# Performance work log

Hardware: AMD Instinct MI355X
Metric: run time of the kernel (lower is better)

## Reference

```python
import jax, jax.numpy as jnp
import numpy as np

E = 1024
H = 16
HD = E // H
FF = 4 * E
B, T = 2, 2048


def _linear_params(key, fan_in, fan_out):
    k1, k2 = jax.random.split(key)
    bound = 1.0 / np.sqrt(fan_in)
    W = jax.random.uniform(k1, (fan_out, fan_in), jnp.float32, -bound, bound)
    b = jax.random.uniform(k2, (fan_out,), jnp.float32, -bound, bound)
    return W, b


def setup_inputs() -> dict:
    key = jax.random.key(0)
    keys = jax.random.split(key, 8)
    x = jax.random.normal(keys[0], (B, T, E), jnp.float32)
    Wq, bq = _linear_params(keys[1], E, E)
    Wk, bk = _linear_params(keys[2], E, E)
    Wv, bv = _linear_params(keys[3], E, E)
    Wo, bo = _linear_params(keys[4], E, E)
    W1, b1 = _linear_params(keys[5], E, FF)
    W2, b2 = _linear_params(keys[6], FF, E)
    ln1_g = jnp.ones((E,), jnp.float32); ln1_b = jnp.zeros((E,), jnp.float32)
    ln2_g = jnp.ones((E,), jnp.float32); ln2_b = jnp.zeros((E,), jnp.float32)
    return {"x": x, "Wq": Wq, "bq": bq, "Wk": Wk, "bk": bk, "Wv": Wv, "bv": bv,
            "Wo": Wo, "bo": bo, "W1": W1, "b1": b1, "W2": W2, "b2": b2,
            "ln1_g": ln1_g, "ln1_b": ln1_b, "ln2_g": ln2_g, "ln2_b": ln2_b}


def _layernorm(x, g, b, eps=1e-5):
    mu = jnp.mean(x, axis=-1, keepdims=True)
    var = jnp.var(x, axis=-1, keepdims=True)
    return (x - mu) * jax.lax.rsqrt(var + eps) * g + b


def reference(x, Wq, bq, Wk, bk, Wv, bv, Wo, bo, W1, b1, W2, b2,
              ln1_g, ln1_b, ln2_g, ln2_b):
    Bc, Tc, Ec = x.shape
    h = _layernorm(x, ln1_g, ln1_b)
    # projections (torch Linear: y = x @ W.T + b)
    q = (h @ Wq.T + bq).reshape(Bc, Tc, H, HD).transpose(0, 2, 1, 3)  # [B,H,T,hd]
    k = (h @ Wk.T + bk).reshape(Bc, Tc, H, HD).transpose(0, 2, 1, 3)
    v = (h @ Wv.T + bv).reshape(Bc, Tc, H, HD).transpose(0, 2, 1, 3)
    scores = jnp.einsum('bhqd,bhkd->bhqk', q, k) / np.sqrt(HD).astype(np.float32)
    causal = jnp.tril(jnp.ones((Tc, Tc), bool))
    scores = jnp.where(causal, scores, -jnp.inf)
    att = jax.nn.softmax(scores, axis=-1)  # dropout = identity (eval)
    out = jnp.einsum('bhqk,bhkd->bhqd', att, v)
    out = out.transpose(0, 2, 1, 3).reshape(Bc, Tc, Ec)
    x = x + out @ Wo.T + bo
    h2 = _layernorm(x, ln2_g, ln2_b)
    ff = jax.nn.relu(h2 @ W1.T + b1) @ W2.T + b2
    return x + ff
```

## Files before the change

### kernel.cpp

```cpp
#include <hip/hip_runtime.h>

typedef unsigned short u16;
typedef __bf16 bf16x8 __attribute__((ext_vector_type(8)));
typedef float f32x4 __attribute__((ext_vector_type(4)));

#define E_ 1024
#define T_ 2048
#define B_ 2
#define H_ 16
#define FF_ 4096
#define M_ 4096

__device__ __forceinline__ u16 f2b(float f) {
    union { float f; unsigned u; } c; c.f = f;
    unsigned r = c.u + 0x7FFFu + ((c.u >> 16) & 1u);
    return (u16)(r >> 16);
}
__device__ __forceinline__ u16 f2bt(float f) {
    union { float f; unsigned u; } c; c.f = f;
    return (u16)(c.u >> 16);
}

__device__ __forceinline__ void gl16(const u16* g, u16* l) {
    __builtin_amdgcn_global_load_lds(
        (__attribute__((address_space(1))) void*)g,
        (__attribute__((address_space(3))) void*)l, 16, 0, 0);
}

template<int N> __device__ __forceinline__ void wait_vmcnt() {
    if constexpr (N == 2)      asm volatile("s_waitcnt vmcnt(2)" ::: "memory");
    else if constexpr (N == 3) asm volatile("s_waitcnt vmcnt(3)" ::: "memory");
    else if constexpr (N == 4) asm volatile("s_waitcnt vmcnt(4)" ::: "memory");
    else                       asm volatile("s_waitcnt vmcnt(0)" ::: "memory");
}

__global__ __launch_bounds__(256) void cvt_ln(
        const float* __restrict__ Wq, const float* __restrict__ Wk,
        const float* __restrict__ Wv, const float* __restrict__ Wo,
        const float* __restrict__ W1, const float* __restrict__ W2,
        const float* __restrict__ bq, const float* __restrict__ bk,
        const float* __restrict__ bv,
        u16* __restrict__ WqkvB, u16* __restrict__ WoB,
        u16* __restrict__ W1B, u16* __restrict__ W2B,
        float* __restrict__ bqkv,
        const float* __restrict__ x, const float* __restrict__ g1,
        const float* __restrict__ b1v, u16* __restrict__ hB) {
    if (blockIdx.x < 1024) {
        int row = blockIdx.x * 4 + (threadIdx.x >> 6);
        int t = threadIdx.x & 63;
        const float* xr = x + (size_t)row * E_;
        float v[16];
        float sum = 0.f, ss = 0.f;
#pragma unroll
        for (int c = 0; c < 4; c++) {
            float4 f = *(const float4*)&xr[c * 256 + t * 4];
            v[c * 4 + 0] = f.x; v[c * 4 + 1] = f.y; v[c * 4 + 2] = f.z; v[c * 4 + 3] = f.w;
            sum += f.x + f.y + f.z + f.w;
            ss += f.x * f.x + f.y * f.y + f.z * f.z + f.w * f.w;
        }
#pragma unroll
        for (int d = 32; d; d >>= 1) {
            sum += __shfl_xor(sum, d);
            ss  += __shfl_xor(ss, d);
        }
        float mu = sum * (1.f / E_);
        float var = ss * (1.f / E_) - mu * mu;
        float rs = rsqrtf(var + 1e-5f);
#pragma unroll
        for (int c = 0; c < 4; c++) {
            int idx = c * 256 + t * 4;
            float4 g4 = *(const float4*)&g1[idx];
            float4 b4 = *(const float4*)&b1v[idx];
            ushort4 o;
            o.x = f2b((v[c * 4 + 0] - mu) * rs * g4.x + b4.x);
            o.y = f2b((v[c * 4 + 1] - mu) * rs * g4.y + b4.y);
            o.z = f2b((v[c * 4 + 2] - mu) * rs * g4.z + b4.z);
            o.w = f2b((v[c * 4 + 3] - mu) * rs * g4.w + b4.w);
            *(ushort4*)&hB[(size_t)row * E_ + idx] = o;
        }
        return;
    }
    int i = (blockIdx.x - 1024) * 256 + threadIdx.x;
    if (i >= 3146496) return;
    if (i >= 3145728) {
        int j = i - 3145728;
        const float* s = (j < 256) ? bq : (j < 512) ? bk : bv;
        int jj = j & 255;
        *(float4*)&bqkv[j * 4] = *(const float4*)&s[jj * 4];
        return;
    }
    const float* src; u16* dst; int j;
    if (i < 786432) {
        src = (i < 262144) ? Wq : (i < 524288) ? Wk : Wv;
        j = i & 262143;
        dst = WqkvB + (i >> 18) * (E_ * E_);
    } else if (i < 1048576) { j = i - 786432;  src = Wo; dst = WoB; }
    else if (i < 2097152)   { j = i - 1048576; src = W1; dst = W1B; }
    else                    { j = i - 2097152; src = W2; dst = W2B; }
    float4 f = *(const float4*)&src[j * 4];
    ushort4 o;
    o.x = f2b(f.x); o.y = f2b(f.y); o.z = f2b(f.z); o.w = f2b(f.w);
    *(ushort4*)&dst[j * 4] = o;
}

__global__ __launch_bounds__(64) void ln_fwd(u16* __restrict__ out, const float* __restrict__ x,
                                             const float* __restrict__ g, const float* __restrict__ bta) {
    int row = blockIdx.x;
    int t = threadIdx.x;
    const float* xr = x + (size_t)row * E_;
    float v[16];
    float sum = 0.f, ss = 0.f;
#pragma unroll
    for (int c = 0; c < 4; c++) {
        float4 f = *(const float4*)&xr[c * 256 + t * 4];
        v[c * 4 + 0] = f.x; v[c * 4 + 1] = f.y; v[c * 4 + 2] = f.z; v[c * 4 + 3] = f.w;
        sum += f.x + f.y + f.z + f.w;
        ss += f.x * f.x + f.y * f.y + f.z * f.z + f.w * f.w;
    }
#pragma unroll
    for (int d = 32; d; d >>= 1) {
        sum += __shfl_xor(sum, d);
        ss  += __shfl_xor(ss, d);
    }
    float mu = sum * (1.f / E_);
    float var = ss * (1.f / E_) - mu * mu;
    float rs = rsqrtf(var + 1e-5f);
#pragma unroll
    for (int c = 0; c < 4; c++) {
        int idx = c * 256 + t * 4;
        float4 g4 = *(const float4*)&g[idx];
        float4 b4 = *(const float4*)&bta[idx];
        ushort4 o;
        o.x = f2b((v[c * 4 + 0] - mu) * rs * g4.x + b4.x);
        o.y = f2b((v[c * 4 + 1] - mu) * rs * g4.y + b4.y);
        o.z = f2b((v[c * 4 + 2] - mu) * rs * g4.z + b4.z);
        o.w = f2b((v[c * 4 + 3] - mu) * rs * g4.w + b4.w);
        *(ushort4*)&out[(size_t)row * E_ + idx] = o;
    }
}

template<int BM, int BN>
__global__ __launch_bounds__(256) void gemm_bt(
        const u16* __restrict__ A, const u16* __restrict__ Bt,
        const float* __restrict__ bias, const float* __restrict__ residual,
        float* __restrict__ outF, float* __restrict__ oP1,
        float* __restrict__ oP2, float* __restrict__ oP3,
        u16* __restrict__ outB, u16* __restrict__ outVt,
        int M, int N, int K, int ldk, int relu, int qkvmode, int swz) {
    constexpr int MT = BM / 32, NT = BN / 32;
    constexpr int LA = BM / 64, LB = BN / 64;
    __shared__ __align__(16) u16 As[3][BM * 32];
    __shared__ __align__(16) u16 Bs[3][BN * 32];
    int tid = threadIdx.x;
    int bx = blockIdx.x, by = blockIdx.y;
    if (swz) {
        int gx = gridDim.x;
        int nwg = gx * gridDim.y;
        int lin = by * gx + bx;
        int w = (lin & 7) * (nwg >> 3) + (lin >> 3);
        bx = w % gx; by = w / gx;
    }
    int m0 = by * BM, n0 = bx * BN;
    int kz = blockIdx.z;
    int koff = kz * K;
    int wave = tid >> 6, lane = tid & 63;
    int wm = wave & 1, wn = wave >> 1;
    int r16 = lane & 15, kg = lane >> 4;

    const u16* gA = A + (size_t)(m0 + wave * (BM / 4) + (lane >> 2)) * ldk + koff + (lane & 3) * 8;
    const u16* gB = Bt + (size_t)(n0 + wave * (BN / 4) + (lane >> 2)) * ldk + koff + (lane & 3) * 8;
    size_t row16 = (size_t)16 * ldk;
    int aoff = wave * (BM / 4) * 32;
    int boff = wave * (BN / 4) * 32;

    f32x4 acc[MT][NT] = {};

    const int nk = K >> 5;

    auto issue = [&](int kt, int buf) {
        int k1 = kt << 5;
        gl16(gA + k1, As[buf] + aoff);
        if (LA == 2) gl16(gA + k1 + row16, As[buf] + aoff + 512);
        gl16(gB + k1, Bs[buf] + boff);
        if (LB == 2) gl16(gB + k1 + row16, Bs[buf] + boff + 512);
    };

    auto compute = [&](int cb) {
        bf16x8 af[MT], bfr[NT];
#pragma unroll
        for (int mt = 0; mt < MT; mt++)
            af[mt] = *(const bf16x8*)&As[cb][(wm * (BM / 2) + mt * 16 + r16) * 32 + kg * 8];
#pragma unroll
        for (int nt = 0; nt < NT; nt++)
            bfr[nt] = *(const bf16x8*)&Bs[cb][(wn * (BN / 2) + nt * 16 + r16) * 32 + kg * 8];
#pragma unroll
        for (int mt = 0; mt < MT; mt++)
#pragma unroll
            for (int nt = 0; nt < NT; nt++)
                acc[mt][nt] = __builtin_amdgcn_mfma_f32_16x16x32_bf16(af[mt], bfr[nt], acc[mt][nt], 0, 0, 0);
    };

    issue(0, 0);
    issue(1, 1);

    int cur = 0;
    for (int ks = 0; ks < nk - 1; ks++) {
        wait_vmcnt<LA + LB>();
        __builtin_amdgcn_s_barrier();
        asm volatile("" ::: "memory");
        if (ks + 2 < nk) {
            int p2 = cur ? cur - 1 : 2;
            issue(ks + 2, p2);
        }
        compute(cur);
        cur = (cur < 2) ? cur + 1 : 0;
    }
    asm volatile("s_waitcnt vmcnt(0)" ::: "memory");
    __builtin_amdgcn_s_barrier();
    asm volatile("" ::: "memory");
    compute(cur);

#pragma unroll
    for (int mt = 0; mt < MT; mt++) {
#pragma unroll
        for (int nt = 0; nt < NT; nt++) {
            int gm = m0 + wm * (BM / 2) + mt * 16 + kg * 4;
            int gn = n0 + wn * (BN / 2) + nt * 16 + r16;
            float bv = bias[gn];
            if (qkvmode) {
                if (gn < 2048) {
                    float scl = (gn < 1024) ? 0.18033688f : 1.0f;
#pragma unroll
                    for (int r = 0; r < 4; r++)
                        outB[(size_t)(gm + r) * 2048 + gn] = f2b((acc[mt][nt][r] + bv) * scl);
                } else {
                    int bq_ = gm >> 11, tq = gm & 2047, d = gn - 2048;
                    ushort4 ov;
                    ov.x = f2b(acc[mt][nt][0] + bv);
                    ov.y = f2b(acc[mt][nt][1] + bv);
                    ov.z = f2b(acc[mt][nt][2] + bv);
                    ov.w = f2b(acc[mt][nt][3] + bv);
                    *(ushort4*)&outVt[((size_t)(bq_ * 1024 + d)) * 2048 + tq] = ov;
                }
            } else if (oP1) {
                float* po = (kz == 1) ? oP1 : (kz == 2) ? oP2 : oP3;
#pragma unroll
                for (int r = 0; r < 4; r++) {
                    size_t off = (size_t)(gm + r) * N + gn;
                    if (kz == 0) {
                        float v = acc[mt][nt][r] + bv;
                        if (residual) v += residual[off];
                        outF[off] = v;
                    } else {
                        po[off] = acc[mt][nt][r];
                    }
                }
            } else {
#pragma unroll
                for (int r = 0; r < 4; r++) {
                    float v = acc[mt][nt][r] + bv;
                    size_t off = (size_t)(gm + r) * N + gn;
                    if (residual) v += residual[off];
                    if (relu) v = fmaxf(v, 0.f);
                    if (outF) outF[off] = v;
                    else outB[off] = f2b(v);
                }
            }
        }
    }
}

__global__ __launch_bounds__(256) void addf3(float* __restrict__ d, const float* __restrict__ a,
                                             const float* __restrict__ b, const float* __restrict__ c) {
    size_t i = ((size_t)blockIdx.x * 256 + threadIdx.x) * 4;
    float4 vd = *(float4*)&d[i];
    float4 va = *(const float4*)&a[i];
    float4 vb = *(const float4*)&b[i];
    float4 vc = *(const float4*)&c[i];
    vd.x += va.x + vb.x + vc.x;
    vd.y += va.y + vb.y + vc.y;
    vd.z += va.z + vb.z + vc.z;
    vd.w += va.w + vb.w + vc.w;
    *(float4*)&d[i] = vd;
}

#define AST 68
__global__ __launch_bounds__(256) void attn_mfma(
        const u16* __restrict__ qk, const u16* __restrict__ vt,
        u16* __restrict__ out) {
    __shared__ __align__(16) u16 Ks[2][64 * AST];
    __shared__ __align__(16) u16 Vs[2][64 * AST];
    __shared__ __align__(16) u16 Ps[4][16 * AST];

    int bz = blockIdx.x;
    int h  = bz & 15;
    int b  = (bz >> 4) & 1;
    int qt = bz >> 5;

    int tid = threadIdx.x;
    int w = tid >> 6, lane = tid & 63;
    int g = lane >> 4, l16 = lane & 15;

    int qrow = qt * 64 + w * 16 + l16;
    bf16x8 qf[2];
    qf[0] = *(const bf16x8*)&qk[(size_t)(b * T_ + qrow) * 2048 + h * 64 + g * 8];
    qf[1] = *(const bf16x8*)&qk[(size_t)(b * T_ + qrow) * 2048 + h * 64 + 32 + g * 8];

    f32x4 o[4] = {};
    f32x4 lp = {0.f, 0.f, 0.f, 0.f};

    int r1 = tid >> 3, col1 = (tid & 7) * 8;
    const u16* gK = qk + (size_t)(b * T_) * 2048 + 1024 + h * 64;
    const u16* gV = vt + (size_t)(b * 1024 + h * 64) * 2048;

    uint4 kr1 = *(const uint4*)&gK[(size_t)r1 * 2048 + col1];
    uint4 kr2 = *(const uint4*)&gK[(size_t)(r1 + 32) * 2048 + col1];
    uint4 vr1 = *(const uint4*)&gV[(size_t)r1 * 2048 + col1];
    uint4 vr2 = *(const uint4*)&gV[(size_t)(r1 + 32) * 2048 + col1];

    for (int t = 0; t <= qt; t++) {
        int cur = t & 1;
        *(uint4*)&Ks[cur][r1 * AST + col1] = kr1;
        *(uint4*)&Ks[cur][(r1 + 32) * AST + col1] = kr2;
        *(uint4*)&Vs[cur][r1 * AST + col1] = vr1;
        *(uint4*)&Vs[cur][(r1 + 32) * AST + col1] = vr2;
        __syncthreads();
        if (t < qt) {
            int j1 = (t + 1) * 64;
            kr1 = *(const uint4*)&gK[(size_t)(j1 + r1) * 2048 + col1];
            kr2 = *(const uint4*)&gK[(size_t)(j1 + r1 + 32) * 2048 + col1];
            vr1 = *(const uint4*)&gV[(size_t)r1 * 2048 + j1 + col1];
            vr2 = *(const uint4*)&gV[(size_t)(r1 + 32) * 2048 + j1 + col1];
        }

        f32x4 s[4];
#pragma unroll
        for (int nt = 0; nt < 4; nt++) {
            f32x4 c16 = {-16.f, -16.f, -16.f, -16.f};
            bf16x8 k0 = *(const bf16x8*)&Ks[cur][(nt * 16 + l16) * AST + g * 8];
            bf16x8 k1 = *(const bf16x8*)&Ks[cur][(nt * 16 + l16) * AST + 32 + g * 8];
            s[nt] = __builtin_amdgcn_mfma_f32_16x16x32_bf16(qf[0], k0, c16, 0, 0, 0);
            s[nt] = __builtin_amdgcn_mfma_f32_16x16x32_bf16(qf[1], k1, s[nt], 0, 0, 0);
        }

        if (t == qt) {
            int j0 = t * 64;
#pragma unroll
            for (int nt = 0; nt < 4; nt++) {
                int key = j0 + nt * 16 + l16;
#pragma unroll
                for (int r = 0; r < 4; r++) {
                    int q = qt * 64 + w * 16 + g * 4 + r;
                    if (key > q) s[nt][r] = -INFINITY;
                }
            }
        }

#pragma unroll
        for (int nt = 0; nt < 4; nt++)
#pragma unroll
            for (int r = 0; r < 4; r++) {
                float p = exp2f(s[nt][r]);
                lp[r] += p;
                Ps[w][(g * 4 + r) * AST + nt * 16 + l16] = f2bt(p);
            }

#pragma unroll
        for (int kf = 0; kf < 2; kf++) {
            bf16x8 pf = *(const bf16x8*)&Ps[w][l16 * AST + kf * 32 + g * 8];
#pragma unroll
            for (int nt = 0; nt < 4; nt++) {
                bf16x8 vf = *(const bf16x8*)&Vs[cur][(nt * 16 + l16) * AST + kf * 32 + g * 8];
                o[nt] = __builtin_amdgcn_mfma_f32_16x16x32_bf16(pf, vf, o[nt], 0, 0, 0);
            }
        }
    }

#pragma unroll
    for (int x = 1; x <= 8; x <<= 1)
#pragma unroll
        for (int r = 0; r < 4; r++)
            lp[r] += __shfl_xor(lp[r], x);

    float inv[4];
#pragma unroll
    for (int r = 0; r < 4; r++) inv[r] = 1.f / lp[r];
    int qg = qt * 64 + w * 16 + g * 4;
#pragma unroll
    for (int nt = 0; nt < 4; nt++)
#pragma unroll
        for (int r = 0; r < 4; r++)
            out[(size_t)(b * T_ + qg + r) * E_ + h * 64 + nt * 16 + l16] =
                f2b(o[nt][r] * inv[r]);
}

extern "C" void kernel_launch(void* const* d_in, const int* in_sizes, int n_in,
                              void* d_out, int out_size, void* d_ws, size_t ws_size,
                              hipStream_t stream) {
    const float* x    = (const float*)d_in[0];
    const float* Wq   = (const float*)d_in[1];
    const float* bq   = (const float*)d_in[2];
    const float* Wk   = (const float*)d_in[3];
    const float* bk   = (const float*)d_in[4];
    const float* Wv   = (const float*)d_in[5];
    const float* bv   = (const float*)d_in[6];
    const float* Wo   = (const float*)d_in[7];
    const float* bo   = (const float*)d_in[8];
    const float* W1   = (const float*)d_in[9];
    const float* b1   = (const float*)d_in[10];
    const float* W2   = (const float*)d_in[11];
    const float* b2   = (const float*)d_in[12];
    const float* ln1g = (const float*)d_in[13];
    const float* ln1b = (const float*)d_in[14];
    const float* ln2g = (const float*)d_in[15];
    const float* ln2b = (const float*)d_in[16];

    char* ws = (char*)d_ws;
    size_t off = 0;
    auto alloc = [&](size_t bytes) { char* p = ws + off; off += (bytes + 255) & ~(size_t)255; return p; };

    u16*   hB    = (u16*)  alloc((size_t)M_ * E_ * 2);
    u16*   WqkvB = (u16*)  alloc((size_t)3 * E_ * E_ * 2);
    u16*   WoB   = (u16*)  alloc((size_t)E_ * E_ * 2);
    u16*   W1B   = (u16*)  alloc((size_t)FF_ * E_ * 2);
    u16*   W2B   = (u16*)  alloc((size_t)E_ * FF_ * 2);
    float* bqkv  = (float*)alloc(3 * E_ * 4);
    u16*   qkB   = (u16*)  alloc((size_t)M_ * 2 * E_ * 2);
    u16*   vtG   = (u16*)  alloc((size_t)M_ * E_ * 2);
    u16*   attnB = (u16*)  alloc((size_t)M_ * E_ * 2);
    float* x2    = (float*)alloc((size_t)M_ * E_ * 4);
    u16*   h2B   = (u16*)  alloc((size_t)M_ * E_ * 2);
    u16*   rB    = (u16*)  alloc((size_t)M_ * FF_ * 2);
    float* P1    = (float*)alloc((size_t)M_ * E_ * 4);
    float* P2 = (float*)qkB;
    float* P3 = (float*)ws;

    cvt_ln<<<1024 + 12291, 256, 0, stream>>>(Wq, Wk, Wv, Wo, W1, W2, bq, bk, bv,
                                             WqkvB, WoB, W1B, W2B, bqkv,
                                             x, ln1g, ln1b, hB);

    gemm_bt<128, 128><<<dim3(3 * E_ / 128, M_ / 128), 256, 0, stream>>>(
        hB, WqkvB, bqkv, nullptr, nullptr, nullptr, nullptr, nullptr, qkB, vtG,
        M_, 3 * E_, E_, E_, 0, 1, 0);

    attn_mfma<<<B_ * H_ * (T_ / 64), 256, 0, stream>>>(qkB, vtG, attnB);

    gemm_bt<64, 128><<<dim3(E_ / 128, M_ / 64), 256, 0, stream>>>(
        attnB, WoB, bo, x, x2, nullptr, nullptr, nullptr, nullptr, nullptr,
        M_, E_, E_, E_, 0, 0, 0);

    ln_fwd<<<M_, 64, 0, stream>>>(h2B, x2, ln2g, ln2b);

    gemm_bt<128, 128><<<dim3(FF_ / 128, M_ / 128), 256, 0, stream>>>(
        h2B, W1B, b1, nullptr, nullptr, nullptr, nullptr, nullptr, rB, nullptr,
        M_, FF_, E_, E_, 1, 0, 1);

    gemm_bt<128, 128><<<dim3(E_ / 128, M_ / 128, 4), 256, 0, stream>>>(
        rB, W2B, b2, x2, (float*)d_out, P1, P2, P3, nullptr, nullptr,
        M_, E_, FF_ / 4, FF_, 0, 0, 1);

    addf3<<<(M_ * E_) / (256 * 4), 256, 0, stream>>>((float*)d_out, P1, P2, P3);
}
```

Baseline: 387.3 us.

## Add 256x256-tile 512-thread GEMM kernel for QKV, FFN1 and FFN2

Introduces a new GEMM kernel with 256x256 output tiles, 8 waves, a K-step of 64, XOR-swizzled LDS layout, double-buffered global-to-LDS loads interleaved across four MFMA phases, and raised wave priority during MFMA. The QKV projection, FFN up-projection and split-K FFN down-projection now use it in place of the 128x128 kernel, aiming for more data reuse per tile and better overlap of loads with compute. The larger tiles mean fewer workgroups (for example 192 for QKV and 64 per split for FFN2), which may underfill the GPU's compute units and raises LDS and register pressure.

```diff
diff --git a/kernel.cpp b/kernel.cpp
--- a/kernel.cpp
+++ b/kernel.cpp
@@ -136,6 +136,155 @@
         o.z = f2b((v[c * 4 + 2] - mu) * rs * g4.z + b4.z);
         o.w = f2b((v[c * 4 + 3] - mu) * rs * g4.w + b4.w);
         *(ushort4*)&out[(size_t)row * E_ + idx] = o;
+    }
+}
+
+template<int QKV, int SPLIT>
+__global__ __launch_bounds__(512) void gemm256(
+        const u16* __restrict__ A, const u16* __restrict__ Bt,
+        const float* __restrict__ bias, const float* __restrict__ residual,
+        float* __restrict__ outF, float* __restrict__ oP1,
+        float* __restrict__ oP2, float* __restrict__ oP3,
+        u16* __restrict__ outB, u16* __restrict__ outVt,
+        int N, int K, int ldk, int relu) {
+    __shared__ __align__(16) u16 As[2][256 * 64];
+    __shared__ __align__(16) u16 Bs[2][256 * 64];
+    int tid = threadIdx.x;
+    int bx = blockIdx.x, by = blockIdx.y;
+    {
+        int gx = gridDim.x;
+        int nwg = gx * (int)gridDim.y, cpx = nwg >> 3;
+        int lin = by * gx + bx;
+        int wv = (lin & 7) * cpx + (lin >> 3);
+        bx = wv % gx; by = wv / gx;
+    }
+    int m0 = by * 256, n0 = bx * 256;
+    int kz = blockIdx.z;
+    int koff = kz * K;
+    int w = tid >> 6, lane = tid & 63;
+    int wm = w >> 2, wn = w & 3;
+    int r16 = lane & 15, kg = lane >> 4;
+    int sw = (r16 & 7) << 3;
+
+    int srow = tid >> 3;
+    int schunk = (tid & 7) ^ (srow & 7);
+    const u16* gAs = A + (size_t)(m0 + srow) * ldk + koff + schunk * 8;
+    const u16* gBs = Bt + (size_t)(n0 + srow) * ldk + koff + schunk * 8;
+    size_t rstep = (size_t)64 * ldk;
+
+    f32x4 acc[8][4] = {};
+    const int nk = K >> 6;
+
+    auto stA = [&](int kt, int b, int r0, int r1) {
+        const u16* g = gAs + kt * 64;
+        u16* l = &As[b][0] + tid * 8;
+        gl16(g + (size_t)r0 * rstep, l + r0 * 4096);
+        gl16(g + (size_t)r1 * rstep, l + r1 * 4096);
+    };
+    auto stB = [&](int kt, int b, int r0, int r1) {
+        const u16* g = gBs + kt * 64;
+        u16* l = &Bs[b][0] + tid * 8;
+        gl16(g + (size_t)r0 * rstep, l + r0 * 4096);
+        gl16(g + (size_t)r1 * rstep, l + r1 * 4096);
+    };
+
+    stB(0, 0, 0, 1); stB(0, 0, 2, 3); stA(0, 0, 0, 2); stA(0, 0, 1, 3);
+    asm volatile("s_waitcnt vmcnt(2)" ::: "memory");
+    __builtin_amdgcn_s_barrier();
+    asm volatile("" ::: "memory");
+
+    for (int t = 0; t < nk; t++) {
+        int cb = t & 1, nb = cb ^ 1;
+        const bool pf = (t + 1 < nk);
+        bf16x8 bfr[4];
+#pragma unroll
+        for (int ph = 0; ph < 4; ph++) {
+            const int kk = ph >> 1, mh = ph & 1;
+            int ce = kk * 32 + kg * 8;
+            if (mh == 0) {
+#pragma unroll
+                for (int nf = 0; nf < 4; nf++) {
+                    int row = wn * 64 + nf * 16 + r16;
+                    bfr[nf] = *(const bf16x8*)&Bs[cb][(row * 64 + ce) ^ sw];
+                }
+            }
+            bf16x8 af[4];
+#pragma unroll
+            for (int i = 0; i < 4; i++) {
+                int row = wm * 128 + (mh * 4 + i) * 16 + r16;
+                af[i] = *(const bf16x8*)&As[cb][(row * 64 + ce) ^ sw];
+            }
+            if (pf) {
+                if (ph == 0)      stB(t + 1, nb, 0, 1);
+                else if (ph == 1) stB(t + 1, nb, 2, 3);
+                else if (ph == 2) stA(t + 1, nb, 0, 2);
+                else              stA(t + 1, nb, 1, 3);
+            }
+            __builtin_amdgcn_s_barrier();
+            asm volatile("s_waitcnt lgkmcnt(0)" ::: "memory");
+            __builtin_amdgcn_s_setprio(1);
+#pragma unroll
+            for (int i = 0; i < 4; i++)
+#pragma unroll
+                for (int nf = 0; nf < 4; nf++)
+                    acc[mh * 4 + i][nf] = __builtin_amdgcn_mfma_f32_16x16x32_bf16(
+                        af[i], bfr[nf], acc[mh * 4 + i][nf], 0, 0, 0);
+            __builtin_amdgcn_s_setprio(0);
+            if (ph == 0) {
+                if (pf) asm volatile("s_waitcnt vmcnt(2)" ::: "memory");
+                else    asm volatile("s_waitcnt vmcnt(0)" ::: "memory");
+            } else if (ph == 3 && pf) {
+                asm volatile("s_waitcnt vmcnt(2)" ::: "memory");
+            }
+            __builtin_amdgcn_s_barrier();
+            asm volatile("" ::: "memory");
+        }
+    }
+
+#pragma unroll
+    for (int mf = 0; mf < 8; mf++) {
+#pragma unroll
+        for (int nf = 0; nf < 4; nf++) {
+            int gm = m0 + wm * 128 + mf * 16 + kg * 4;
+            int gn = n0 + wn * 64 + nf * 16 + r16;
+            float bv = bias[gn];
+            if (QKV) {
+                if (gn < 2048) {
+                    float scl = (gn < 1024) ? 0.18033688f : 1.0f;
+#pragma unroll
+                    for (int r = 0; r < 4; r++)
+                        outB[(size_t)(gm + r) * 2048 + gn] = f2b((acc[mf][nf][r] + bv) * scl);
+                } else {
+                    int bq_ = gm >> 11, tq = gm & 2047, d = gn - 2048;
+                    ushort4 ov;
+                    ov.x = f2b(acc[mf][nf][0] + bv);
+                    ov.y = f2b(acc[mf][nf][1] + bv);
+                    ov.z = f2b(acc[mf][nf][2] + bv);
+                    ov.w = f2b(acc[mf][nf][3] + bv);
+                    *(ushort4*)&outVt[((size_t)(bq_ * 1024 + d)) * 2048 + tq] = ov;
+                }
+            } else if (SPLIT) {
+                float* po = (kz == 1) ? oP1 : (kz == 2) ? oP2 : oP3;
+#pragma unroll
+                for (int r = 0; r < 4; r++) {
+                    size_t off = (size_t)(gm + r) * N + gn;
+                    if (kz == 0) {
+                        float v = acc[mf][nf][r] + bv;
+                        if (residual) v += residual[off];
+                        outF[off] = v;
+                    } else {
+                        po[off] = acc[mf][nf][r];
+                    }
+                }
+            } else {
+#pragma unroll
+                for (int r = 0; r < 4; r++) {
+                    float v = acc[mf][nf][r] + bv;
+                    if (relu) v = fmaxf(v, 0.f);
+                    outB[(size_t)(gm + r) * N + gn] = f2b(v);
+                }
+            }
+        }
     }
 }
 
@@ -157,8 +306,8 @@
         int gx = gridDim.x;
         int nwg = gx * gridDim.y;
         int lin = by * gx + bx;
-        int w = (lin & 7) * (nwg >> 3) + (lin >> 3);
-        bx = w % gx; by = w / gx;
+        int wv = (lin & 7) * (nwg >> 3) + (lin >> 3);
+        bx = wv % gx; by = wv / gx;
     }
     int m0 = by * BM, n0 = bx * BN;
     int kz = blockIdx.z;
@@ -439,9 +588,9 @@
                                              WqkvB, WoB, W1B, W2B, bqkv,
                                              x, ln1g, ln1b, hB);
 
-    gemm_bt<128, 128><<<dim3(3 * E_ / 128, M_ / 128), 256, 0, stream>>>(
-        hB, WqkvB, bqkv, nullptr, nullptr, nullptr, nullptr, nullptr, qkB, vtG,
-        M_, 3 * E_, E_, E_, 0, 1, 0);
+    gemm256<1, 0><<<dim3(3 * E_ / 256, M_ / 256), 512, 0, stream>>>(
+        hB, WqkvB, bqkv, nullptr, nullptr, nullptr, nullptr, nullptr,
+        qkB, vtG, 3 * E_, E_, E_, 0);
 
     attn_mfma<<<B_ * H_ * (T_ / 64), 256, 0, stream>>>(qkB, vtG, attnB);
 
@@ -451,13 +600,13 @@
 
     ln_fwd<<<M_, 64, 0, stream>>>(h2B, x2, ln2g, ln2b);
 
-    gemm_bt<128, 128><<<dim3(FF_ / 128, M_ / 128), 256, 0, stream>>>(
-        h2B, W1B, b1, nullptr, nullptr, nullptr, nullptr, nullptr, rB, nullptr,
-        M_, FF_, E_, E_, 1, 0, 1);
-
-    gemm_bt<128, 128><<<dim3(E_ / 128, M_ / 128, 4), 256, 0, stream>>>(
-        rB, W2B, b2, x2, (float*)d_out, P1, P2, P3, nullptr, nullptr,
-        M_, E_, FF_ / 4, FF_, 0, 0, 1);
+    gemm256<0, 0><<<dim3(FF_ / 256, M_ / 256), 512, 0, stream>>>(
+        h2B, W1B, b1, nullptr, nullptr, nullptr, nullptr, nullptr,
+        rB, nullptr, FF_, E_, E_, 1);
+
+    gemm256<0, 1><<<dim3(E_ / 256, M_ / 256, 4), 512, 0, stream>>>(
+        rB, W2B, b2, x2, (float*)d_out, P1, P2, P3,
+        nullptr, nullptr, E_, FF_ / 4, FF_, 0);
 
     addf3<<<(M_ * E_) / (256 * 4), 256, 0, stream>>>((float*)d_out, P1, P2, P3);
 }
```

After: 392.1 us. About the same (+1.2%).
